# Kernel optimization log

Measured on AMD Instinct MI355X. Metric: run time of the kernel, lower is better.

Reference implementation:

```python
import jax, jax.numpy as jnp
import numpy as np

S, B, C, H, W_SP = 2, 16, 256, 64, 64
K = 3

def setup_inputs() -> dict:
    key = jax.random.key(0)
    k1, k2 = jax.random.split(key)
    x = jax.random.normal(k1, (S, B, C, H, W_SP), dtype=jnp.float32)
    W = jax.random.normal(k2, (C, C, K, K), dtype=jnp.float32) * 0.05
    return {"x": x, "W": W}

def reference(x, W):
    shape = x.shape
    C_ = shape[-3]
    k = W.shape[-1]
    pad = k // 2
    # flatten leading dims -> (N, C, H, W)
    xf = x.reshape((-1,) + shape[-3:])
    # diagonal mask: zero out all cross-channel filters (effectively depthwise)
    eye = jnp.eye(C_, dtype=W.dtype)[:, :, None, None]
    w = W * eye
    out = jax.lax.conv_general_dilated(
        xf, w,
        window_strides=(1, 1),
        padding=[(pad, pad), (pad, pad)],
        dimension_numbers=("NCHW", "OIHW", "NCHW"),
    )
    return out.reshape(shape)
```

## Files before the change

### kernel.cpp

```cpp
#include <hip/hip_runtime.h>


#define C_CH 256
#define H_SP 64
#define W_SP 64
#define PLANE (H_SP * W_SP)

typedef float f32x4 __attribute__((ext_vector_type(4)));

__global__ __launch_bounds__(256) void dwconv3x3_direct(
    const float* __restrict__ x,
    const float* __restrict__ Wfull,
    float* __restrict__ out)
{
    const int p = blockIdx.x;
    const int c = p & (C_CH - 1);
    const float* __restrict__ xp = x + (size_t)p * PLANE;
    float* __restrict__ op = out + (size_t)p * PLANE;

    const float* __restrict__ wp = Wfull + (size_t)c * (C_CH + 1) * 9;
    const float w00 = wp[0], w01 = wp[1], w02 = wp[2];
    const float w10 = wp[3], w11 = wp[4], w12 = wp[5];
    const float w20 = wp[6], w21 = wp[7], w22 = wp[8];

    const int t = threadIdx.x;

#pragma unroll
    for (int i = 0; i < 4; ++i) {
        const int f  = t + i * 256;
        const int h  = f >> 4;
        const int w4 = (f & 15) << 2;

        float acx = 0.f, acy = 0.f, acz = 0.f, acw = 0.f;

#pragma unroll
        for (int kh = 0; kh < 3; ++kh) {
            const int hh = h + kh - 1;
            if (hh < 0 || hh >= H_SP) continue;
            const float* __restrict__ row = xp + hh * W_SP;

            const float4 v  = *(const float4*)(row + w4);
            const float cm1 = (w4 > 0)        ? row[w4 - 1] : 0.f;
            const float c4  = (w4 < W_SP - 4) ? row[w4 + 4] : 0.f;

            float k0, k1, k2;
            if (kh == 0)      { k0 = w00; k1 = w01; k2 = w02; }
            else if (kh == 1) { k0 = w10; k1 = w11; k2 = w12; }
            else              { k0 = w20; k1 = w21; k2 = w22; }

            acx += cm1 * k0 + v.x * k1 + v.y * k2;
            acy += v.x * k0 + v.y * k1 + v.z * k2;
            acz += v.y * k0 + v.z * k1 + v.w * k2;
            acw += v.z * k0 + v.w * k1 + c4  * k2;
        }

        f32x4 acc = { acx, acy, acz, acw };
        __builtin_nontemporal_store(acc, (f32x4*)(op) + f);
    }
}

extern "C" void kernel_launch(void* const* d_in, const int* in_sizes, int n_in,
                              void* d_out, int out_size, void* d_ws, size_t ws_size,
                              hipStream_t stream) {
    const float* x = (const float*)d_in[0];
    const float* W = (const float*)d_in[1];
    float* out = (float*)d_out;

    const int n_planes = out_size / PLANE;
    dwconv3x3_direct<<<n_planes, 256, 0, stream>>>(x, W, out);
}
```

Baseline: 269.4 us.

## Stage per-wave row bands in LDS and use lane shuffles for horizontal halo

Each wavefront now loads a 16-row band plus two halo rows of the plane into shared memory once, with coalesced float4 loads. It then reads the three input rows per output row from LDS instead of global memory. Left and right neighbor pixels come from cross-lane shuffles rather than extra scalar global loads. This cuts redundant global and cache traffic and load instruction count, at the cost of LDS usage and shuffle instructions. It relies on wave-local ordering with no block barrier.

After: 229.9 us. 14.6% less time.

```diff
diff --git a/kernel.cpp b/kernel.cpp
--- a/kernel.cpp
+++ b/kernel.cpp
@@ -5,31 +5,69 @@
 #define H_SP 64
 #define W_SP 64
 #define PLANE (H_SP * W_SP)
+#define BAND_ROWS 18
 
 typedef float f32x4 __attribute__((ext_vector_type(4)));
 
-__global__ __launch_bounds__(256) void dwconv3x3_direct(
+__global__ __launch_bounds__(256) void dwconv3x3_band2(
     const float* __restrict__ x,
     const float* __restrict__ Wfull,
     float* __restrict__ out)
 {
-    const int p = blockIdx.x;
-    const int c = p & (C_CH - 1);
+    __shared__ float lds[4 * BAND_ROWS * W_SP];
+
+    const int tid  = threadIdx.x;
+    const int wid  = tid >> 6;
+    const int lane = tid & 63;
+    const int rr   = lane >> 4;
+    const int cc   = lane & 15;
+
+    const int p  = blockIdx.x;
+    const int c  = p & (C_CH - 1);
+    const int r0 = wid << 4;
+
     const float* __restrict__ xp = x + (size_t)p * PLANE;
-    float* __restrict__ op = out + (size_t)p * PLANE;
+    float* __restrict__ op       = out + (size_t)p * PLANE;
 
     const float* __restrict__ wp = Wfull + (size_t)c * (C_CH + 1) * 9;
     const float w00 = wp[0], w01 = wp[1], w02 = wp[2];
     const float w10 = wp[3], w11 = wp[4], w12 = wp[5];
     const float w20 = wp[6], w21 = wp[7], w22 = wp[8];
 
-    const int t = threadIdx.x;
+    float* tile = &lds[wid * BAND_ROWS * W_SP];
+
+    float4 v0, v1, v2, v3;
+    {
+        int g0 = r0 - 1 + rr;       g0 = g0 < 0 ? 0 : g0;
+        int g1 = r0 + 3 + rr;
+        int g2 = r0 + 7 + rr;
+        int g3 = r0 + 11 + rr;      g3 = g3 > H_SP - 1 ? H_SP - 1 : g3;
+        const int co = cc << 2;
+        v0 = *(const float4*)(xp + g0 * W_SP + co);
+        v1 = *(const float4*)(xp + g1 * W_SP + co);
+        v2 = *(const float4*)(xp + g2 * W_SP + co);
+        v3 = *(const float4*)(xp + g3 * W_SP + co);
+    }
+    float h0, h1;
+    {
+        int g4 = r0 + 15;
+        int g5 = r0 + 16;           g5 = g5 > H_SP - 1 ? H_SP - 1 : g5;
+        h0 = xp[g4 * W_SP + lane];
+        h1 = xp[g5 * W_SP + lane];
+    }
+    {
+        const int co = cc << 2;
+        *(float4*)(tile + (rr     ) * W_SP + co) = v0;
+        *(float4*)(tile + (rr +  4) * W_SP + co) = v1;
+        *(float4*)(tile + (rr +  8) * W_SP + co) = v2;
+        *(float4*)(tile + (rr + 12) * W_SP + co) = v3;
+        tile[16 * W_SP + lane] = h0;
+        tile[17 * W_SP + lane] = h1;
+    }
 
 #pragma unroll
-    for (int i = 0; i < 4; ++i) {
-        const int f  = t + i * 256;
-        const int h  = f >> 4;
-        const int w4 = (f & 15) << 2;
+    for (int s = 0; s < 4; ++s) {
+        const int h = r0 + 4 * s + rr;
 
         float acx = 0.f, acy = 0.f, acz = 0.f, acw = 0.f;
 
@@ -37,25 +75,27 @@
         for (int kh = 0; kh < 3; ++kh) {
             const int hh = h + kh - 1;
             if (hh < 0 || hh >= H_SP) continue;
-            const float* __restrict__ row = xp + hh * W_SP;
+            const int lh = hh - r0 + 1;
 
-            const float4 v  = *(const float4*)(row + w4);
-            const float cm1 = (w4 > 0)        ? row[w4 - 1] : 0.f;
-            const float c4  = (w4 < W_SP - 4) ? row[w4 + 4] : 0.f;
+            const f32x4 v = *(const f32x4*)(tile + lh * W_SP + (cc << 2));
+            float left  = __shfl_up(v.w, 1);
+            float right = __shfl_down(v.x, 1);
+            if (cc == 0)  left  = 0.f;
+            if (cc == 15) right = 0.f;
 
             float k0, k1, k2;
             if (kh == 0)      { k0 = w00; k1 = w01; k2 = w02; }
             else if (kh == 1) { k0 = w10; k1 = w11; k2 = w12; }
             else              { k0 = w20; k1 = w21; k2 = w22; }
 
-            acx += cm1 * k0 + v.x * k1 + v.y * k2;
-            acy += v.x * k0 + v.y * k1 + v.z * k2;
-            acz += v.y * k0 + v.z * k1 + v.w * k2;
-            acw += v.z * k0 + v.w * k1 + c4  * k2;
+            acx += left * k0 + v.x * k1 + v.y * k2;
+            acy += v.x  * k0 + v.y * k1 + v.z * k2;
+            acz += v.y  * k0 + v.z * k1 + v.w * k2;
+            acw += v.z  * k0 + v.w * k1 + right * k2;
         }
 
         f32x4 acc = { acx, acy, acz, acw };
-        __builtin_nontemporal_store(acc, (f32x4*)(op) + f);
+        __builtin_nontemporal_store(acc, (f32x4*)op + (h << 4) + cc);
     }
 }
 
@@ -67,5 +107,5 @@
     float* out = (float*)d_out;
 
     const int n_planes = out_size / PLANE;
-    dwconv3x3_direct<<<n_planes, 256, 0, stream>>>(x, W, out);
+    dwconv3x3_band2<<<n_planes, 256, 0, stream>>>(x, W, out);
 }
```
